# Kernel optimization log

Hardware: AMD Instinct MI355X
Metric: run time of the kernel (lower is better)

Reference implementation:

```python
import jax, jax.numpy as jnp
import numpy as np

NUM_BINS = 15
NUM_CLASSES = 4
NEIGHBORHOOD_WIDTH = 3  # K; num_neighbor_classes = K**2 = 9


def _neighbor_counts(onehot):
    """Count of same-class neighbors in KxK window (center excluded), zero padding.
    onehot: [B, C, H, W] float32 one-hot of hard predictions.
    returns int32 [B, C, H, W] in [0, K^2-1].
    """
    K = NEIGHBORHOOD_WIDTH
    C = onehot.shape[1]
    kern = np.ones((K, K), dtype=np.float32)
    kern[K // 2, K // 2] = 0.0  # exclude center pixel
    kernel = jnp.asarray(np.broadcast_to(kern, (C, 1, K, K)).copy())  # depthwise OIHW
    counts = jax.lax.conv_general_dilated(
        onehot, kernel,
        window_strides=(1, 1), padding='SAME',
        feature_group_count=C,
        dimension_numbers=('NCHW', 'OIHW', 'NCHW'))
    return jnp.clip(jnp.round(counts).astype(jnp.int32), 0, K * K - 1)


def setup_inputs() -> dict:
    key = jax.random.key(0)
    k1, k2 = jax.random.split(key)
    logits = jax.random.normal(k1, (16, NUM_CLASSES, 512, 512), dtype=jnp.float32)
    # calibration frequency table: val_freqs[class][neighbor_count][conf_bin]
    val_freqs = jax.random.uniform(k2, (NUM_CLASSES, NEIGHBORHOOD_WIDTH ** 2, NUM_BINS), dtype=jnp.float32)
    return {"logits": logits, "val_freqs": val_freqs}


def reference(logits, val_freqs):
    B, C, H, W = logits.shape
    probs = jax.nn.softmax(logits, axis=1)                      # [B,C,H,W]
    y_hard = jnp.argmax(probs, axis=1)                          # [B,H,W]

    # (y_hard == lab_idx) for every class at once -> one-hot [B,C,H,W]
    onehot = jax.nn.one_hot(y_hard, C, axis=1, dtype=jnp.float32)
    agg = _neighbor_counts(onehot)                              # [B,C,H,W] int32 in [0, K^2-1]

    # confidence bin per pixel/class: uniform bins on [0,1]
    bin_width = 1.0 / NUM_BINS
    bin_map = jnp.clip((probs / bin_width).astype(jnp.int32), 0, NUM_BINS - 1)  # [B,C,H,W]

    # fused multi-index gather replacing the nested class/neighbor-mask loops:
    # calibrated[b,c,h,w] = val_freqs[c, agg[b,c,h,w], bin_map[b,c,h,w]]
    cls_idx = jnp.arange(C, dtype=jnp.int32)[None, :, None, None]
    calibrated = val_freqs[cls_idx, agg, bin_map]               # [B,C,H,W]

    # normalize across classes, guarding zero sums
    s = jnp.sum(calibrated, axis=1, keepdims=True)
    s = jnp.where(s == 0, 1.0, s)
    return calibrated / s
```

## Files before the change

kernel.cpp:

```cpp
#include <hip/hip_runtime.h>

#define HW (512 * 512)

constexpr int TX = 64, TY = 16;
constexpr int CW = TX + 2;
constexpr int CH = TY + 2;
constexpr float BWIDTH = 1.0f / 15.0f;
constexpr float DELTA = 2e-5f;

__global__ __launch_bounds__(256) void nectar_binning_kernel(
    const float* __restrict__ logits,
    const float* __restrict__ val_freqs,
    float* __restrict__ out)
{
    __shared__ unsigned int cls[CH * CW];
    __shared__ float vf[540];

    const int b  = blockIdx.z;
    const int w0 = blockIdx.x * TX;
    const int h0 = blockIdx.y * TY;
    const int tid = threadIdx.y * 32 + threadIdx.x;

    for (int i = tid; i < 540; i += 256) vf[i] = val_freqs[i];

    const float* lb = logits + (size_t)b * 4 * HW;

    for (int i = tid; i < CH * CW; i += 256) {
        int ly = i / CW;
        int lx = i - ly * CW;
        int hh = h0 + ly - 1;
        int ww = w0 + lx - 1;
        unsigned int v = 0;
        if ((unsigned)hh < 512u && (unsigned)ww < 512u) {
            int base = (hh << 9) + ww;
            float x0 = lb[base];
            float x1 = lb[HW + base];
            float x2 = lb[2 * HW + base];
            float x3 = lb[3 * HW + base];
            int c = 0; float best = x0;
            if (x1 > best) { best = x1; c = 1; }
            if (x2 > best) { best = x2; c = 2; }
            if (x3 > best) { best = x3; c = 3; }
            v = 1u << (4 * c);
        }
        cls[i] = v;
    }
    __syncthreads();

    const int tx = threadIdx.x;
    const int ty = threadIdx.y;
    const int w  = w0 + 2 * tx;
    const int h  = h0 + 2 * ty;

    float x[2][4][2];
    #pragma unroll
    for (int jy = 0; jy < 2; jy++) {
        int base = ((h + jy) << 9) + w;
        #pragma unroll
        for (int c = 0; c < 4; c++) {
            float2 v = *reinterpret_cast<const float2*>(lb + (size_t)c * HW + base);
            x[jy][c][0] = v.x; x[jy][c][1] = v.y;
        }
    }

    unsigned int rowv[4][4];
    #pragma unroll
    for (int r = 0; r < 4; r++) {
        const unsigned int* rp = &cls[(2 * ty + r) * CW + 2 * tx];
        rowv[r][0] = rp[0]; rowv[r][1] = rp[1]; rowv[r][2] = rp[2]; rowv[r][3] = rp[3];
    }
    unsigned int coltop[4], colbot[4];
    #pragma unroll
    for (int j = 0; j < 4; j++) {
        unsigned int mid = rowv[1][j] + rowv[2][j];
        coltop[j] = mid + rowv[0][j];
        colbot[j] = mid + rowv[3][j];
    }
    unsigned int packed[2][2];
    packed[0][0] = coltop[0] + coltop[1] + coltop[2] - rowv[1][1];
    packed[0][1] = coltop[1] + coltop[2] + coltop[3] - rowv[1][2];
    packed[1][0] = colbot[0] + colbot[1] + colbot[2] - rowv[2][1];
    packed[1][1] = colbot[1] + colbot[2] + colbot[3] - rowv[2][2];

    float* ob = out + (size_t)b * 4 * HW;

    #pragma unroll
    for (int jy = 0; jy < 2; jy++) {
        float res[2][4];
        #pragma unroll
        for (int jx = 0; jx < 2; jx++) {
            float x0 = x[jy][0][jx], x1 = x[jy][1][jx], x2 = x[jy][2][jx], x3 = x[jy][3][jx];
            float m = fmaxf(fmaxf(x0, x1), fmaxf(x2, x3));
            float e[4];
            e[0] = expf(x0 - m); e[1] = expf(x1 - m);
            e[2] = expf(x2 - m); e[3] = expf(x3 - m);
            float s = ((e[0] + e[1]) + e[2]) + e[3];

            float rs = __builtin_amdgcn_rcpf(s);
            float q[4];
            bool slow = false;
            #pragma unroll
            for (int c = 0; c < 4; c++) {
                q[c] = (e[c] * rs) * 15.0f;
                float f = q[c] - floorf(q[c]);
                slow |= (f < DELTA) | (f > 1.0f - DELTA);
            }
            if (slow) {
                #pragma unroll
                for (int c = 0; c < 4; c++) q[c] = (e[c] / s) / BWIDTH;
            }

            unsigned int pk = packed[jy][jx];
            float cs = 0.0f;
            float cal[4];
            #pragma unroll
            for (int c = 0; c < 4; c++) {
                int bin = (int)q[c];
                bin = bin > 14 ? 14 : bin;
                int cnt = (int)((pk >> (4 * c)) & 0xFu);
                float v = vf[c * 135 + cnt * 15 + bin];
                cal[c] = v;
                cs += v;
            }
            if (cs == 0.0f) cs = 1.0f;
            float inv = __builtin_amdgcn_rcpf(cs);
            #pragma unroll
            for (int c = 0; c < 4; c++) res[jx][c] = cal[c] * inv;
        }
        int base = ((h + jy) << 9) + w;
        #pragma unroll
        for (int c = 0; c < 4; c++) {
            float2 v; v.x = res[0][c]; v.y = res[1][c];
            *reinterpret_cast<float2*>(ob + (size_t)c * HW + base) = v;
        }
    }
}

extern "C" void kernel_launch(void* const* d_in, const int* in_sizes, int n_in,
                              void* d_out, int out_size, void* d_ws, size_t ws_size,
                              hipStream_t stream) {
    const float* logits    = (const float*)d_in[0];
    const float* val_freqs = (const float*)d_in[1];
    float* out             = (float*)d_out;

    dim3 block(32, 8, 1);
    dim3 grid(512 / TX, 512 / TY, 16);
    hipLaunchKernelGGL(nectar_binning_kernel, grid, block, 0, stream,
                       logits, val_freqs, out);
}
```

Baseline: 129.7 us.

## Load interior logits once in float4 per thread, halo-only staging, nontemporal stores

Each thread now loads a 1x4 strip of logits with float4 loads and computes argmax, softmax and bins from registers before the barrier. Only the 164 halo cells are loaded separately into shared memory, so interior logits are no longer read twice. Output uses float4 nontemporal stores, the fast path uses __expf, and DELTA is widened to preserve exactness checks with the less precise exp. This trades more registers per thread and a different LDS stride for fewer global loads.

```diff
diff --git a/kernel.cpp b/kernel.cpp
--- a/kernel.cpp
+++ b/kernel.cpp
@@ -2,137 +2,146 @@
 
 #define HW (512 * 512)
 
+typedef float vfloat4 __attribute__((ext_vector_type(4)));
+
 constexpr int TX = 64, TY = 16;
-constexpr int CW = TX + 2;
-constexpr int CH = TY + 2;
+constexpr int CWP = 67;
 constexpr float BWIDTH = 1.0f / 15.0f;
-constexpr float DELTA = 2e-5f;
+constexpr float DELTA = 3e-5f;
 
 __global__ __launch_bounds__(256) void nectar_binning_kernel(
     const float* __restrict__ logits,
     const float* __restrict__ val_freqs,
     float* __restrict__ out)
 {
-    __shared__ unsigned int cls[CH * CW];
+    __shared__ unsigned int cls[18 * CWP];
     __shared__ float vf[540];
 
     const int b  = blockIdx.z;
     const int w0 = blockIdx.x * TX;
     const int h0 = blockIdx.y * TY;
-    const int tid = threadIdx.y * 32 + threadIdx.x;
+    const int tid = threadIdx.x;
 
     for (int i = tid; i < 540; i += 256) vf[i] = val_freqs[i];
 
     const float* lb = logits + (size_t)b * 4 * HW;
 
-    for (int i = tid; i < CH * CW; i += 256) {
-        int ly = i / CW;
-        int lx = i - ly * CW;
+    const int tix = tid & 15;
+    const int tiy = tid >> 4;
+    const int w = w0 + 4 * tix;
+    const int h = h0 + tiy;
+    const int base = (h << 9) + w;
+
+    float xv[4][4];
+    #pragma unroll
+    for (int c = 0; c < 4; c++) {
+        vfloat4 v = *reinterpret_cast<const vfloat4*>(lb + (size_t)c * HW + base);
+        xv[c][0] = v.x; xv[c][1] = v.y; xv[c][2] = v.z; xv[c][3] = v.w;
+    }
+
+    unsigned int pbin[4];
+    #pragma unroll
+    for (int j = 0; j < 4; j++) {
+        float x0 = xv[0][j], x1 = xv[1][j], x2 = xv[2][j], x3 = xv[3][j];
+        int c = 0; float best = x0;
+        if (x1 > best) { best = x1; c = 1; }
+        if (x2 > best) { best = x2; c = 2; }
+        if (x3 > best) { best = x3; c = 3; }
+        cls[(tiy + 1) * CWP + 1 + 4 * tix + j] = 1u << (4 * c);
+
+        float m = fmaxf(fmaxf(x0, x1), fmaxf(x2, x3));
+        float t0 = x0 - m, t1 = x1 - m, t2 = x2 - m, t3 = x3 - m;
+        float f0 = __expf(t0), f1 = __expf(t1), f2 = __expf(t2), f3 = __expf(t3);
+        float sf = ((f0 + f1) + f2) + f3;
+        float rs = __builtin_amdgcn_rcpf(sf);
+        float q[4];
+        q[0] = (f0 * rs) * 15.0f; q[1] = (f1 * rs) * 15.0f;
+        q[2] = (f2 * rs) * 15.0f; q[3] = (f3 * rs) * 15.0f;
+        bool slow = false;
+        #pragma unroll
+        for (int c2 = 0; c2 < 4; c2++) {
+            float fr = q[c2] - floorf(q[c2]);
+            slow |= (fr < DELTA) | (fr > 1.0f - DELTA);
+        }
+        if (slow) {
+            float e0 = expf(t0), e1 = expf(t1), e2 = expf(t2), e3 = expf(t3);
+            float s = ((e0 + e1) + e2) + e3;
+            q[0] = (e0 / s) / BWIDTH; q[1] = (e1 / s) / BWIDTH;
+            q[2] = (e2 / s) / BWIDTH; q[3] = (e3 / s) / BWIDTH;
+        }
+        unsigned int pb = 0;
+        #pragma unroll
+        for (int c2 = 0; c2 < 4; c2++) {
+            int bin = (int)q[c2];
+            bin = bin > 14 ? 14 : bin;
+            pb |= (unsigned int)bin << (4 * c2);
+        }
+        pbin[j] = pb;
+    }
+
+    if (tid < 164) {
+        int ly, lx;
+        if (tid < 66)       { ly = 0;        lx = tid;       }
+        else if (tid < 132) { ly = 17;       lx = tid - 66;  }
+        else if (tid < 148) { ly = tid - 131; lx = 0;        }
+        else                { ly = tid - 147; lx = 65;       }
         int hh = h0 + ly - 1;
         int ww = w0 + lx - 1;
         unsigned int v = 0;
         if ((unsigned)hh < 512u && (unsigned)ww < 512u) {
-            int base = (hh << 9) + ww;
-            float x0 = lb[base];
-            float x1 = lb[HW + base];
-            float x2 = lb[2 * HW + base];
-            float x3 = lb[3 * HW + base];
+            int bb = (hh << 9) + ww;
+            float x0 = lb[bb];
+            float x1 = lb[HW + bb];
+            float x2 = lb[2 * HW + bb];
+            float x3 = lb[3 * HW + bb];
             int c = 0; float best = x0;
             if (x1 > best) { best = x1; c = 1; }
             if (x2 > best) { best = x2; c = 2; }
             if (x3 > best) { best = x3; c = 3; }
             v = 1u << (4 * c);
         }
-        cls[i] = v;
+        cls[ly * CWP + lx] = v;
     }
     __syncthreads();
 
-    const int tx = threadIdx.x;
-    const int ty = threadIdx.y;
-    const int w  = w0 + 2 * tx;
-    const int h  = h0 + 2 * ty;
+    const unsigned int* p0 = &cls[tiy * CWP + 4 * tix];
+    unsigned int r1[6], colsum[6];
+    #pragma unroll
+    for (int j = 0; j < 6; j++) {
+        unsigned int a = p0[j];
+        unsigned int bmid = p0[CWP + j];
+        unsigned int cbot = p0[2 * CWP + j];
+        r1[j] = bmid;
+        colsum[j] = a + bmid + cbot;
+    }
 
-    float x[2][4][2];
+    float res[4][4];
     #pragma unroll
-    for (int jy = 0; jy < 2; jy++) {
-        int base = ((h + jy) << 9) + w;
+    for (int j = 0; j < 4; j++) {
+        unsigned int pk = colsum[j] + colsum[j + 1] + colsum[j + 2] - r1[j + 1];
+        unsigned int pb = pbin[j];
+        float cs = 0.0f;
+        float cal[4];
         #pragma unroll
         for (int c = 0; c < 4; c++) {
-            float2 v = *reinterpret_cast<const float2*>(lb + (size_t)c * HW + base);
-            x[jy][c][0] = v.x; x[jy][c][1] = v.y;
+            int cnt = (int)((pk >> (4 * c)) & 0xFu);
+            int bin = (int)((pb >> (4 * c)) & 0xFu);
+            float v = vf[c * 135 + cnt * 15 + bin];
+            cal[c] = v;
+            cs += v;
         }
+        if (cs == 0.0f) cs = 1.0f;
+        float inv = __builtin_amdgcn_rcpf(cs);
+        #pragma unroll
+        for (int c = 0; c < 4; c++) res[c][j] = cal[c] * inv;
     }
 
-    unsigned int rowv[4][4];
+    float* ob = out + (size_t)b * 4 * HW + base;
     #pragma unroll
-    for (int r = 0; r < 4; r++) {
-        const unsigned int* rp = &cls[(2 * ty + r) * CW + 2 * tx];
-        rowv[r][0] = rp[0]; rowv[r][1] = rp[1]; rowv[r][2] = rp[2]; rowv[r][3] = rp[3];
-    }
-    unsigned int coltop[4], colbot[4];
-    #pragma unroll
-    for (int j = 0; j < 4; j++) {
-        unsigned int mid = rowv[1][j] + rowv[2][j];
-        coltop[j] = mid + rowv[0][j];
-        colbot[j] = mid + rowv[3][j];
-    }
-    unsigned int packed[2][2];
-    packed[0][0] = coltop[0] + coltop[1] + coltop[2] - rowv[1][1];
-    packed[0][1] = coltop[1] + coltop[2] + coltop[3] - rowv[1][2];
-    packed[1][0] = colbot[0] + colbot[1] + colbot[2] - rowv[2][1];
-    packed[1][1] = colbot[1] + colbot[2] + colbot[3] - rowv[2][2];
-
-    float* ob = out + (size_t)b * 4 * HW;
-
-    #pragma unroll
-    for (int jy = 0; jy < 2; jy++) {
-        float res[2][4];
-        #pragma unroll
-        for (int jx = 0; jx < 2; jx++) {
-            float x0 = x[jy][0][jx], x1 = x[jy][1][jx], x2 = x[jy][2][jx], x3 = x[jy][3][jx];
-            float m = fmaxf(fmaxf(x0, x1), fmaxf(x2, x3));
-            float e[4];
-            e[0] = expf(x0 - m); e[1] = expf(x1 - m);
-            e[2] = expf(x2 - m); e[3] = expf(x3 - m);
-            float s = ((e[0] + e[1]) + e[2]) + e[3];
-
-            float rs = __builtin_amdgcn_rcpf(s);
-            float q[4];
-            bool slow = false;
-            #pragma unroll
-            for (int c = 0; c < 4; c++) {
-                q[c] = (e[c] * rs) * 15.0f;
-                float f = q[c] - floorf(q[c]);
-                slow |= (f < DELTA) | (f > 1.0f - DELTA);
-            }
-            if (slow) {
-                #pragma unroll
-                for (int c = 0; c < 4; c++) q[c] = (e[c] / s) / BWIDTH;
-            }
-
-            unsigned int pk = packed[jy][jx];
-            float cs = 0.0f;
-            float cal[4];
-            #pragma unroll
-            for (int c = 0; c < 4; c++) {
-                int bin = (int)q[c];
-                bin = bin > 14 ? 14 : bin;
-                int cnt = (int)((pk >> (4 * c)) & 0xFu);
-                float v = vf[c * 135 + cnt * 15 + bin];
-                cal[c] = v;
-                cs += v;
-            }
-            if (cs == 0.0f) cs = 1.0f;
-            float inv = __builtin_amdgcn_rcpf(cs);
-            #pragma unroll
-            for (int c = 0; c < 4; c++) res[jx][c] = cal[c] * inv;
-        }
-        int base = ((h + jy) << 9) + w;
-        #pragma unroll
-        for (int c = 0; c < 4; c++) {
-            float2 v; v.x = res[0][c]; v.y = res[1][c];
-            *reinterpret_cast<float2*>(ob + (size_t)c * HW + base) = v;
-        }
+    for (int c = 0; c < 4; c++) {
+        vfloat4 v;
+        v.x = res[c][0]; v.y = res[c][1]; v.z = res[c][2]; v.w = res[c][3];
+        __builtin_nontemporal_store(v, reinterpret_cast<vfloat4*>(ob + (size_t)c * HW));
     }
 }
 
@@ -143,7 +152,7 @@
     const float* val_freqs = (const float*)d_in[1];
     float* out             = (float*)d_out;
 
-    dim3 block(32, 8, 1);
+    dim3 block(256, 1, 1);
     dim3 grid(512 / TX, 512 / TY, 16);
     hipLaunchKernelGGL(nectar_binning_kernel, grid, block, 0, stream,
                        logits, val_freqs, out);
```

Measured after the change: 118.2 us. 8.8% less time.
